# Optimization experiments

Hardware: AMD Instinct MI355X
Metric: run time of the kernel (lower is better)

## Reference

```python
import jax, jax.numpy as jnp
import numpy as np

B, T_ENC, T_DEC = 32, 600, 600
TARGET, PRE, HID, ATT, LOCF, LOCK, POSTH = 80, 256, 512, 128, 32, 31, 512


def _lstm(x, h, c, wih, whh, bih, bhh):
    g = x @ wih.T + bih + h @ whh.T + bhh
    i, f, gg, o = jnp.split(g, 4, axis=-1)
    c2 = jax.nn.sigmoid(f) * c + jax.nn.sigmoid(i) * jnp.tanh(gg)
    return jax.nn.sigmoid(o) * jnp.tanh(c2), c2


def _conv1d(x, w, pad):
    return jax.lax.conv_general_dilated(x, w, (1,), [(pad, pad)], dimension_numbers=('NCH', 'OIH', 'NCH'))


def setup_inputs():
    key = jax.random.key(0)
    ks = jax.random.split(key, 24)
    rn = lambda k, s: jax.random.normal(k, s, dtype=jnp.float32) * 0.05
    return {
        'encoder_inputs': jax.random.normal(ks[0], (B, T_ENC, HID), dtype=jnp.float32),
        'decoder_inputs': jax.random.normal(ks[1], (B, T_DEC, TARGET), dtype=jnp.float32),
        'pn_w1': rn(ks[2], (PRE, TARGET)), 'pn_b1': jnp.zeros((PRE,), jnp.float32),
        'pn_w2': rn(ks[3], (PRE, PRE)), 'pn_b2': jnp.zeros((PRE,), jnp.float32),
        'arnn_wih': rn(ks[4], (4 * HID, PRE + HID)), 'arnn_whh': rn(ks[5], (4 * HID, HID)),
        'arnn_bih': jnp.zeros((4 * HID,), jnp.float32), 'arnn_bhh': jnp.zeros((4 * HID,), jnp.float32),
        'drnn_wih': rn(ks[6], (4 * HID, 2 * HID)), 'drnn_whh': rn(ks[7], (4 * HID, HID)),
        'drnn_bih': jnp.zeros((4 * HID,), jnp.float32), 'drnn_bhh': jnp.zeros((4 * HID,), jnp.float32),
        'mem_w': rn(ks[8], (ATT, HID)), 'mem_b': jnp.zeros((ATT,), jnp.float32),
        'q_w': rn(ks[9], (ATT, HID)),
        'loc_conv_w': rn(ks[10], (LOCF, 2, LOCK)),
        'loc_fc_w': rn(ks[11], (ATT, LOCF)),
        'v_w': rn(ks[12], (1, ATT)),
        'proj_w': rn(ks[13], (TARGET, 2 * HID)),
        'post_w0': rn(ks[14], (POSTH, TARGET, 5)), 'post_b0': jnp.zeros((POSTH,), jnp.float32),
        'post_w1': rn(ks[15], (POSTH, POSTH, 5)), 'post_b1': jnp.zeros((POSTH,), jnp.float32),
        'post_w2': rn(ks[16], (POSTH, POSTH, 5)), 'post_b2': jnp.zeros((POSTH,), jnp.float32),
        'post_w3': rn(ks[17], (POSTH, POSTH, 5)), 'post_b3': jnp.zeros((POSTH,), jnp.float32),
        'post_w4': rn(ks[18], (TARGET, POSTH, 5)), 'post_b4': jnp.zeros((TARGET,), jnp.float32),
    }


def _forward(encoder_inputs, decoder_inputs, pn_w1, pn_b1, pn_w2, pn_b2,
             arnn_wih, arnn_whh, arnn_bih, arnn_bhh,
             drnn_wih, drnn_whh, drnn_bih, drnn_bhh,
             mem_w, mem_b, q_w, loc_conv_w, loc_fc_w, v_w, proj_w,
             post_w0, post_b0, post_w1, post_b1, post_w2, post_b2,
             post_w3, post_b3, post_w4, post_b4):
    Bsz, Tdec, tdim = decoder_inputs.shape
    Tenc = encoder_inputs.shape[1]
    dt = decoder_inputs.dtype
    # prenet on [go_frame; decoder_inputs]; loop consumes frames 0..Tdec-1
    go = jnp.zeros((Bsz, 1, tdim), dt)
    dec = jnp.concatenate([go, decoder_inputs], axis=1)
    pre = jax.nn.relu(jax.nn.relu(dec @ pn_w1.T + pn_b1) @ pn_w2.T + pn_b2)
    xs = jnp.transpose(pre[:, :Tdec], (1, 0, 2))  # (Tdec, B, PRE)
    proc_mem = encoder_inputs @ mem_w.T + mem_b  # (B, Tenc, ATT)
    z = jnp.zeros((Bsz, HID), dt)
    zw = jnp.zeros((Bsz, Tenc), dt)
    carry0 = (z, z, z, z, z, zw, zw)

    def step(carry, dec_in):
        ah, ac, dh, dc, ctx, w, wcum = carry
        ah, ac = _lstm(jnp.concatenate([dec_in, ctx], -1), ah, ac, arnn_wih, arnn_whh, arnn_bih, arnn_bhh)
        wcat = jnp.stack([w, wcum], axis=1)  # (B, 2, Tenc)
        loc = _conv1d(wcat, loc_conv_w, (LOCK - 1) // 2)  # (B, LOCF, Tenc)
        loc = jnp.einsum('bct,ac->bta', loc, loc_fc_w)  # (B, Tenc, ATT)
        q = ah @ q_w.T  # (B, ATT)
        e = jnp.tanh(q[:, None, :] + proc_mem + loc) @ v_w[0]  # (B, Tenc)
        w2 = jax.nn.softmax(e, axis=-1)
        ctx2 = jnp.einsum('bt,bte->be', w2, encoder_inputs)
        wcum2 = wcum + w2
        dh2, dc2 = _lstm(jnp.concatenate([ah, ctx2], -1), dh, dc, drnn_wih, drnn_whh, drnn_bih, drnn_bhh)
        mel = jnp.concatenate([dh2, ctx2], -1) @ proj_w.T  # (B, TARGET)
        return (ah, ac, dh2, dc2, ctx2, w2, wcum2), mel

    _, mels = jax.lax.scan(step, carry0, xs)
    mel_out = jnp.transpose(mels, (1, 0, 2))  # (B, Tdec, TARGET)
    # postnet: 5 conv1d layers, tanh on all but last (eval mode, no dropout)
    y = jnp.transpose(mel_out, (0, 2, 1))  # (B, TARGET, Tdec)
    y = jnp.tanh(_conv1d(y, post_w0, 2) + post_b0[None, :, None])
    y = jnp.tanh(_conv1d(y, post_w1, 2) + post_b1[None, :, None])
    y = jnp.tanh(_conv1d(y, post_w2, 2) + post_b2[None, :, None])
    y = jnp.tanh(_conv1d(y, post_w3, 2) + post_b3[None, :, None])
    y = _conv1d(y, post_w4, 2) + post_b4[None, :, None]  # (B, TARGET, Tdec)
    return mel_out + jnp.transpose(y, (0, 2, 1))


def reference(encoder_inputs, decoder_inputs, pn_w1, pn_b1, pn_w2, pn_b2,
              arnn_wih, arnn_whh, arnn_bih, arnn_bhh,
              drnn_wih, drnn_whh, drnn_bih, drnn_bhh,
              mem_w, mem_b, q_w, loc_conv_w, loc_fc_w, v_w, proj_w,
              post_w0, post_b0, post_w1, post_b1, post_w2, post_b2,
              post_w3, post_b3, post_w4, post_b4):
    return _forward(encoder_inputs, decoder_inputs, pn_w1, pn_b1, pn_w2, pn_b2,
                    arnn_wih, arnn_whh, arnn_bih, arnn_bhh,
                    drnn_wih, drnn_whh, drnn_bih, drnn_bhh,
                    mem_w, mem_b, q_w, loc_conv_w, loc_fc_w, v_w, proj_w,
                    post_w0, post_b0, post_w1, post_b1, post_w2, post_b2,
                    post_w3, post_b3, post_w4, post_b4)
```

## Files before the change

kernel.cpp:

```cpp
#include <hip/hip_runtime.h>
#include <hip/hip_bf16.h>

typedef __hip_bfloat16 bf16;

#define NB   32
#define TE   600
#define TD   600
#define TGT  80
#define PREN 256
#define HID  512
#define ATTD 128
#define LF   32
#define LK   31
#define PH   512

__device__ __forceinline__ float b2f(bf16 x){ return __bfloat162float(x); }

__device__ __forceinline__ void ld8bf(const bf16* p, float* o){
  const uint4 u = *(const uint4*)p;
  o[0]=__uint_as_float(u.x<<16); o[1]=__uint_as_float(u.x&0xFFFF0000u);
  o[2]=__uint_as_float(u.y<<16); o[3]=__uint_as_float(u.y&0xFFFF0000u);
  o[4]=__uint_as_float(u.z<<16); o[5]=__uint_as_float(u.z&0xFFFF0000u);
  o[6]=__uint_as_float(u.w<<16); o[7]=__uint_as_float(u.w&0xFFFF0000u);
}

__device__ __forceinline__ void ld8f(const float* p, float* o){
  float4 a=*(const float4*)p, b=*(const float4*)(p+4);
  o[0]=a.x;o[1]=a.y;o[2]=a.z;o[3]=a.w;
  o[4]=b.x;o[5]=b.y;o[6]=b.z;o[7]=b.w;
}

__device__ __forceinline__ float dot8(const float* w, const float* z){
  return w[0]*z[0]+w[1]*z[1]+w[2]*z[2]+w[3]*z[3]
       + w[4]*z[4]+w[5]*z[5]+w[6]*z[6]+w[7]*z[7];
}

__device__ __forceinline__ float sigm(float x){ return 1.f/(1.f+__expf(-x)); }
__device__ __forceinline__ float tanhfast(float x){
  float e = __expf(2.f*x);
  return 1.f - 2.f/(e+1.f);
}

__global__ __launch_bounds__(256) void k_prenet(const float* __restrict__ dec,
    const float* __restrict__ w1, const float* __restrict__ b1,
    const float* __restrict__ w2, const float* __restrict__ b2,
    bf16* __restrict__ XS)
{
  int t = blockIdx.x, tid = threadIdx.x;
  __shared__ __align__(16) float fr[NB*TGT];
  __shared__ __align__(16) float h1[NB*PREN];
  for (int i=tid;i<NB*TGT;i+=256){
    int b=i/TGT,c=i%TGT;
    fr[b*TGT+c] = (t==0)?0.f:dec[((size_t)b*TD+(t-1))*TGT+c];
  }
  __syncthreads();
  {
    int oc=tid; float bb=b1[oc];
    const float* wr = w1 + (size_t)oc*TGT;
    for (int b=0;b<NB;b++){
      float acc=bb;
      for (int k=0;k<TGT;k+=8){
        float wv[8]; ld8f(wr+k,wv);
        acc += dot8(wv, fr + b*TGT + k);
      }
      h1[b*PREN+oc]=fmaxf(acc,0.f);
    }
  }
  __syncthreads();
  {
    int oc=tid; float bb=b2[oc];
    const float* wr = w2 + (size_t)oc*PREN;
    for (int b=0;b<NB;b++){
      float acc=bb;
      for (int k=0;k<PREN;k+=8){
        float wv[8]; ld8f(wr+k,wv);
        acc += dot8(wv, h1 + b*PREN + k);
      }
      XS[((size_t)t*NB+b)*PREN+oc]=__float2bfloat16(fmaxf(acc,0.f));
    }
  }
}

__global__ __launch_bounds__(256) void k_procmem(const float* __restrict__ enc,
    const float* __restrict__ mw, const float* __restrict__ mb, bf16* __restrict__ PM)
{
  int t=blockIdx.x, tid=threadIdx.x;
  __shared__ __align__(16) float xe[16*HID];
  int a = tid & 127, bh = tid >> 7;
  float bb = mb[a];
  const float* wr = mw + (size_t)a*HID;
  for (int half=0; half<2; half++){
    __syncthreads();
    for (int i=tid;i<16*HID;i+=256){
      int bl=i>>9, h=i&511;
      xe[i] = enc[((size_t)(half*16+bl)*TE + t)*HID + h];
    }
    __syncthreads();
    for (int bl=bh*8; bl<bh*8+8; bl++){
      float acc=bb;
      for (int k=0;k<HID;k+=8){
        float wv[8]; ld8f(wr+k,wv);
        acc += dot8(wv, xe + bl*HID + k);
      }
      PM[((size_t)(half*16+bl)*TE + t)*ATTD + a] = __float2bfloat16(acc);
    }
  }
}

__global__ __launch_bounds__(256) void k_att1m(
    const float* __restrict__ AHn, const float* __restrict__ W,
    const float* __restrict__ WCUM, const bf16* __restrict__ PM,
    float* __restrict__ E,
    const float* __restrict__ qw, const float* __restrict__ convw,
    const float* __restrict__ fcw, const float* __restrict__ vw,
    const float* __restrict__ DHp, const float* __restrict__ CTX,
    const float* __restrict__ projw, float* __restrict__ MEL, int t)
{
  int blk = blockIdx.x, tid = threadIdx.x;
  int b = blk & 31, chunk = blk >> 5;
  __shared__ __align__(16) float wpad[632], wcpad[632], qs[128], vv[128];
  __shared__ __align__(16) float fcs[128*33];
  __shared__ __align__(16) float cw0[32*31], cw1[32*31];
  __shared__ __align__(16) float convb[4][32];
  for (int i=tid;i<630;i+=256){
    wpad[i]  = (i>=15 && i<615) ? W[(size_t)b*TE + i-15] : 0.f;
    wcpad[i] = (i>=15 && i<615) ? WCUM[(size_t)b*TE + i-15] : 0.f;
  }
  for (int i=tid;i<32*31;i+=256){
    int c=i/31, k=i-c*31;
    cw0[i] = convw[c*62 + k];
    cw1[i] = convw[c*62 + 31 + k];
  }
  for (int i=tid;i<128*33;i+=256){
    int a=i/33, c=i-a*33;
    fcs[i] = (c<32)? fcw[a*32+c] : 0.f;
  }
  if (tid < 128){
    vv[tid] = vw[tid];
    const float* qr = qw + (size_t)tid*HID;
    const float* ah = AHn + b*HID;
    float acc = 0.f;
    for (int k=0;k<HID;k+=8){
      float wv[8]; ld8f(qr+k,wv);
      acc += dot8(wv, ah+k);
    }
    qs[tid] = acc;
  }
  if (t>0 && tid<40){
    int md = blk*5 + (tid>>3);
    int jb = tid&7;
    int o = md%TGT, bb = md/TGT;
    const float* pw = projw + (size_t)o*1024;
    const float* dh = DHp + bb*HID;
    const float* c2 = CTX + bb*HID;
    float a=0.f;
    for (int i=0;i<16;i++){
      int k = jb*128 + i*8;
      const float* zp = (k<512)? dh+k : c2+(k-512);
      float z[8]; ld8f(zp,z);
      float wv[8]; ld8f(pw+k,wv);
      a += dot8(wv,z);
    }
    a += __shfl_xor(a,1); a += __shfl_xor(a,2); a += __shfl_xor(a,4);
    if (jb==0) MEL[((size_t)bb*TD + (t-1))*TGT + o] = a;
  }
  __syncthreads();
  int wid = tid>>6, lane = tid&63;
  int tbase = chunk*38;
  int tend  = min(tbase+38, TE);
  for (int it=0; it<10; it++){
    int tt = tbase + it*4 + wid;
    bool act = (tt < tend);
    if (act && lane < 32){
      int c = lane; float s = 0.f;
      for (int k=0;k<LK;k++)
        s += cw0[c*31+k]*wpad[tt+k] + cw1[c*31+k]*wcpad[tt+k];
      convb[wid][c] = s;
    }
    __syncthreads();
    if (act){
      float part = 0.f;
      #pragma unroll
      for (int half=0; half<2; half++){
        int a = lane + half*64;
        float loc = 0.f;
        #pragma unroll
        for (int c=0;c<32;c++) loc += fcs[a*33+c]*convb[wid][c];
        float x = qs[a] + b2f(PM[((size_t)b*TE + tt)*ATTD + a]) + loc;
        part += vv[a]*tanhfast(x);
      }
      for (int off=1; off<64; off<<=1) part += __shfl_xor(part, off);
      if (lane==0) E[(size_t)b*TE + tt] = part;
    }
    __syncthreads();
  }
}

__global__ __launch_bounds__(256) void k_att23(const float* __restrict__ E,
    float* __restrict__ W, float* __restrict__ WCUM,
    const float* __restrict__ enc, float* __restrict__ CTX)
{
  int blk=blockIdx.x, tid=threadIdx.x;
  int b = blk>>4, q16 = blk&15;
  __shared__ __align__(16) float wl[600];
  __shared__ float part[256];
  __shared__ float red[4];
  float e0[3]; float mx=-1e30f;
  #pragma unroll
  for (int r=0;r<3;r++){
    int i=tid+r*256;
    float v=(i<TE)? E[(size_t)b*TE+i] : -1e30f;
    e0[r]=v; mx=fmaxf(mx,v);
  }
  for (int off=1;off<64;off<<=1) mx=fmaxf(mx,__shfl_xor(mx,off));
  if ((tid&63)==0) red[tid>>6]=mx;
  __syncthreads();
  float m=fmaxf(fmaxf(red[0],red[1]),fmaxf(red[2],red[3]));
  float ex[3]; float s=0.f;
  #pragma unroll
  for (int r=0;r<3;r++){
    int i=tid+r*256;
    ex[r]=(i<TE)? __expf(e0[r]-m) : 0.f;
    s+=ex[r];
  }
  for (int off=1;off<64;off<<=1) s+=__shfl_xor(s,off);
  __syncthreads();
  if ((tid&63)==0) red[tid>>6]=s;
  __syncthreads();
  float inv=1.f/(red[0]+red[1]+red[2]+red[3]);
  #pragma unroll
  for (int r=0;r<3;r++){
    int i=tid+r*256;
    if (i<TE){
      float w2=ex[r]*inv;
      wl[i]=w2;
      if (q16==0){
        W[(size_t)b*TE+i]=w2;
        WCUM[(size_t)b*TE+i]+=w2;
      }
    }
  }
  __syncthreads();
  {
    int hl=tid&31, tj=tid>>5;
    int h=q16*32+hl;
    const float* ep = enc + ((size_t)b*TE)*HID + h;
    int tb_=tj*75;
    float a0=0.f,a1=0.f,a2=0.f;
    for (int u=0;u<25;u++){
      int tt=tb_+u*3;
      a0 += wl[tt  ]*ep[(size_t)(tt  )*HID];
      a1 += wl[tt+1]*ep[(size_t)(tt+1)*HID];
      a2 += wl[tt+2]*ep[(size_t)(tt+2)*HID];
    }
    part[tid]=a0+a1+a2;
  }
  __syncthreads();
  if (tid<32){
    float v=0.f;
    #pragma unroll
    for (int k=0;k<8;k++) v += part[tid + 32*k];
    CTX[b*HID + q16*32 + tid]=v;
  }
}

__global__ __launch_bounds__(256) void k_lstmAD(
    const bf16* __restrict__ XS, const float* __restrict__ CTX,
    float* __restrict__ AH0, float* __restrict__ AH1, float* __restrict__ AC,
    float* __restrict__ DH0, float* __restrict__ DH1, float* __restrict__ DC,
    const float* __restrict__ awih, const float* __restrict__ awhh,
    const float* __restrict__ abih, const float* __restrict__ abhh,
    const float* __restrict__ dwih, const float* __restrict__ dwhh,
    const float* __restrict__ dbih, const float* __restrict__ dbhh,
    int t)
{
  int blk=blockIdx.x, tid=threadIdx.x;
  int b=tid>>3, j=tid&7;
  if (blk<512){
    int s = t+1;
    if (s>=TD) return;
    int cell = blk;
    const bf16* xs = XS + ((size_t)s*NB+b)*PREN;
    const float* cx = CTX + b*HID;
    const float* hr = ((s&1)?AH1:AH0) + b*HID;
    float* hw = (s&1)?AH0:AH1;
    float acc[4];
    #pragma unroll
    for (int q=0;q<4;q++) acc[q]=0.f;
    for (int i=0;i<20;i++){
      int k8=i*64+j*8;
      float z[8];
      if (k8<256) ld8bf(xs+k8,z);
      else ld8f((k8<768)? cx+(k8-256) : hr+(k8-768), z);
      #pragma unroll
      for (int g=0;g<4;g++){
        int row = g*HID + cell;
        const float* wp = (k8<768) ? (awih + (size_t)row*768 + k8)
                                   : (awhh + (size_t)row*HID + (k8-768));
        float wv[8]; ld8f(wp,wv);
        acc[g] += dot8(wv,z);
      }
    }
    #pragma unroll
    for (int q=0;q<4;q++){
      acc[q] += __shfl_xor(acc[q],1);
      acc[q] += __shfl_xor(acc[q],2);
      acc[q] += __shfl_xor(acc[q],4);
    }
    if (j==0){
      float g0=acc[0]+abih[0*HID+cell]+abhh[0*HID+cell];
      float g1=acc[1]+abih[1*HID+cell]+abhh[1*HID+cell];
      float g2=acc[2]+abih[2*HID+cell]+abhh[2*HID+cell];
      float g3=acc[3]+abih[3*HID+cell]+abhh[3*HID+cell];
      float c2 = sigm(g1)*AC[b*HID+cell] + sigm(g0)*tanhfast(g2);
      AC[b*HID+cell]=c2;
      hw[b*HID+cell]=sigm(g3)*tanhfast(c2);
    }
  } else {
    if (t<0) return;
    int cell = blk-512;
    const float* ah  = ((t&1)?AH0:AH1) + b*HID;
    const float* cx  = CTX + b*HID;
    const float* dhr = ((t&1)?DH1:DH0) + b*HID;
    float* dhw = (t&1)?DH0:DH1;
    float acc[4];
    #pragma unroll
    for (int q=0;q<4;q++) acc[q]=0.f;
    for (int i=0;i<24;i++){
      int k8=i*64+j*8;
      const float* zp = (k8<512)? ah+k8 : (k8<1024)? cx+(k8-512) : dhr+(k8-1024);
      float z[8]; ld8f(zp,z);
      #pragma unroll
      for (int g=0;g<4;g++){
        int row = g*HID + cell;
        const float* wp = (k8<1024) ? (dwih + (size_t)row*1024 + k8)
                                    : (dwhh + (size_t)row*HID + (k8-1024));
        float wv[8]; ld8f(wp,wv);
        acc[g] += dot8(wv,z);
      }
    }
    #pragma unroll
    for (int q=0;q<4;q++){
      acc[q] += __shfl_xor(acc[q],1);
      acc[q] += __shfl_xor(acc[q],2);
      acc[q] += __shfl_xor(acc[q],4);
    }
    if (j==0){
      float g0=acc[0]+dbih[0*HID+cell]+dbhh[0*HID+cell];
      float g1=acc[1]+dbih[1*HID+cell]+dbhh[1*HID+cell];
      float g2=acc[2]+dbih[2*HID+cell]+dbhh[2*HID+cell];
      float g3=acc[3]+dbih[3*HID+cell]+dbhh[3*HID+cell];
      float c2 = sigm(g1)*DC[b*HID+cell] + sigm(g0)*tanhfast(g2);
      DC[b*HID+cell]=c2;
      dhw[b*HID+cell]=sigm(g3)*tanhfast(c2);
    }
  }
}

__global__ __launch_bounds__(256) void k_melfinal(const float* __restrict__ DH,
    const float* __restrict__ CTX, const float* __restrict__ projw, float* __restrict__ MEL)
{
  int gid=blockIdx.x*256+threadIdx.x;
  if (gid>=NB*TGT) return;
  int o=gid%TGT, b=gid/TGT;
  const float* pw=projw+(size_t)o*1024;
  float a=0.f;
  for (int k=0;k<HID;k+=8){
    float wv[8]; ld8f(pw+k,wv);
    a += dot8(wv, DH + b*HID + k);
  }
  for (int k=0;k<HID;k+=8){
    float wv[8]; ld8f(pw+512+k,wv);
    a += dot8(wv, CTX + b*HID + k);
  }
  MEL[((size_t)b*TD+599)*TGT+o]=a;
}

__global__ __launch_bounds__(256) void k_conv(
    const void* __restrict__ inv_, bf16* __restrict__ out,
    const float* __restrict__ w, const float* __restrict__ bias,
    int IC, int OC, int mel_in, int do_tanh, int b0)
{
  __shared__ __align__(16) float xs[256*36];
  int bl=blockIdx.x, bg=b0+bl, oct=blockIdx.y, t0=blockIdx.z*32, tid=threadIdx.x;
  int oc = oct*256 + tid;
  float acc[32];
  #pragma unroll
  for (int q=0;q<32;q++) acc[q]=0.f;
  int nch=(IC+255)/256;
  const float* inf_ = (const float*)inv_;
  const bf16*  inb_ = (const bf16*)inv_;
  for (int ch=0;ch<nch;ch++){
    int icb=ch*256, icn=min(256,IC-icb);
    __syncthreads();
    for (int i=tid;i<icn*36;i+=256){
      int icl=i/36, tt=i-icl*36;
      int tg=t0+tt-2;
      float v=0.f;
      if (tg>=0 && tg<TD){
        int ic=icb+icl;
        v = mel_in ? inf_[((size_t)bg*TD+tg)*TGT+ic]
                   : b2f(inb_[((size_t)bl*IC+ic)*TD+tg]);
      }
      xs[i]=v;
    }
    __syncthreads();
    if (oc<OC){
      const float* wp = w + ((size_t)oc*IC+icb)*5;
      for (int ic=0;ic<icn;ic++){
        float xw[36];
        #pragma unroll
        for (int q=0;q<9;q++) ((float4*)xw)[q]=((const float4*)(xs+ic*36))[q];
        float wk0=wp[ic*5  ],wk1=wp[ic*5+1],wk2=wp[ic*5+2],
              wk3=wp[ic*5+3],wk4=wp[ic*5+4];
        #pragma unroll
        for (int tt=0;tt<32;tt++)
          acc[tt] += wk0*xw[tt]+wk1*xw[tt+1]+wk2*xw[tt+2]+wk3*xw[tt+3]+wk4*xw[tt+4];
      }
    }
  }
  if (oc<OC){
    float bv=bias[oc];
    for (int tt=0;tt<32;tt++){
      int tg=t0+tt;
      if (tg<TD){
        float v=acc[tt]+bv;
        if (do_tanh) v=tanhfast(v);
        out[((size_t)bl*OC+oc)*TD+tg]=__float2bfloat16(v);
      }
    }
  }
}

__global__ __launch_bounds__(256) void k_conv_last(
    const bf16* __restrict__ in, const float* __restrict__ w,
    const float* __restrict__ bias, float* __restrict__ outp, int b0)
{
  __shared__ __align__(16) float xs[256*36];
  int bl=blockIdx.x, bg=b0+bl, t0=blockIdx.z*32, tid=threadIdx.x;
  int oc = tid;
  float acc[32];
  #pragma unroll
  for (int q=0;q<32;q++) acc[q]=0.f;
  for (int ch=0;ch<2;ch++){
    int icb=ch*256;
    __syncthreads();
    for (int i=tid;i<256*36;i+=256){
      int icl=i/36, tt=i-icl*36;
      int tg=t0+tt-2;
      float v=0.f;
      if (tg>=0 && tg<TD){
        int ic=icb+icl;
        v = b2f(in[((size_t)bl*PH+ic)*TD+tg]);
      }
      xs[i]=v;
    }
    __syncthreads();
    if (oc<TGT){
      const float* wp = w + ((size_t)oc*PH+icb)*5;
      for (int ic=0;ic<256;ic++){
        float xw[36];
        #pragma unroll
        for (int q=0;q<9;q++) ((float4*)xw)[q]=((const float4*)(xs+ic*36))[q];
        float wk0=wp[ic*5  ],wk1=wp[ic*5+1],wk2=wp[ic*5+2],
              wk3=wp[ic*5+3],wk4=wp[ic*5+4];
        #pragma unroll
        for (int tt=0;tt<32;tt++)
          acc[tt] += wk0*xw[tt]+wk1*xw[tt+1]+wk2*xw[tt+2]+wk3*xw[tt+3]+wk4*xw[tt+4];
      }
    }
  }
  if (oc<TGT){
    float bv=bias[oc];
    for (int tt=0;tt<32;tt++){
      int tg=t0+tt;
      if (tg<TD){
        size_t idx=((size_t)bg*TD+tg)*TGT+oc;
        outp[idx]=acc[tt]+bv+outp[idx];
      }
    }
  }
}

extern "C" void kernel_launch(void* const* d_in, const int* in_sizes, int n_in,
                              void* d_out, int out_size, void* d_ws, size_t ws_size,
                              hipStream_t stream)
{
  const float* enc =(const float*)d_in[0];
  const float* dec =(const float*)d_in[1];
  const float* pw1 =(const float*)d_in[2];  const float* pb1=(const float*)d_in[3];
  const float* pw2 =(const float*)d_in[4];  const float* pb2=(const float*)d_in[5];
  const float* awih=(const float*)d_in[6];  const float* awhh=(const float*)d_in[7];
  const float* abih=(const float*)d_in[8];  const float* abhh=(const float*)d_in[9];
  const float* dwih=(const float*)d_in[10]; const float* dwhh=(const float*)d_in[11];
  const float* dbih=(const float*)d_in[12]; const float* dbhh=(const float*)d_in[13];
  const float* memw=(const float*)d_in[14]; const float* memb=(const float*)d_in[15];
  const float* qw  =(const float*)d_in[16];
  const float* lcw =(const float*)d_in[17];
  const float* lfw =(const float*)d_in[18];
  const float* vw  =(const float*)d_in[19];
  const float* pjw =(const float*)d_in[20];
  const float* cwt0=(const float*)d_in[21]; const float* cbt0=(const float*)d_in[22];
  const float* cwt1=(const float*)d_in[23]; const float* cbt1=(const float*)d_in[24];
  const float* cwt2=(const float*)d_in[25]; const float* cbt2=(const float*)d_in[26];
  const float* cwt3=(const float*)d_in[27]; const float* cbt3=(const float*)d_in[28];
  const float* cwt4=(const float*)d_in[29]; const float* cbt4=(const float*)d_in[30];
  float* MEL = (float*)d_out;
  (void)in_sizes; (void)n_in; (void)out_size; (void)ws_size;

  char* base=(char*)d_ws;
  const size_t XS_B = (size_t)TD*NB*PREN*2;
  const size_t PM_B = (size_t)NB*TE*ATTD*2;
  const size_t HB   = (size_t)NB*HID*4;
  const size_t WB   = (size_t)NB*TE*4;
  bf16* XSb = (bf16*)base;
  bf16* PMb = (bf16*)(base + XS_B);
  char* sbase = base + XS_B + PM_B;
  float* AH0b=(float*)(sbase+0*HB);
  float* AH1b=(float*)(sbase+1*HB);
  float* ACb =(float*)(sbase+2*HB);
  float* DH0b=(float*)(sbase+3*HB);
  float* DH1b=(float*)(sbase+4*HB);
  float* DCb =(float*)(sbase+5*HB);
  float* CTX =(float*)(sbase+6*HB);
  float* Wb  =(float*)(sbase+7*HB);
  float* WC  =(float*)(sbase+7*HB+WB);
  float* Eb  =(float*)(sbase+7*HB+2*WB);
  const int G = 8;
  const size_t PBc_B = (size_t)G*PH*TD*2;
  bf16* PB0 = (bf16*)base;
  bf16* PB1 = (bf16*)(base + PBc_B);

  hipMemsetAsync(sbase, 0, 7*HB+3*WB, stream);

  k_prenet<<<TD,256,0,stream>>>(dec,pw1,pb1,pw2,pb2,XSb);
  k_procmem<<<TE,256,0,stream>>>(enc,memw,memb,PMb);

  k_lstmAD<<<1024,256,0,stream>>>(XSb,CTX,AH0b,AH1b,ACb,DH0b,DH1b,DCb,
                                  awih,awhh,abih,abhh,dwih,dwhh,dbih,dbhh,-1);
  for (int t=0;t<TD;t++){
    const float* AHn = (t&1)? AH0b : AH1b;
    const float* DHp = (t&1)? DH1b : DH0b;
    k_att1m<<<512,256,0,stream>>>(AHn,Wb,WC,PMb,Eb,qw,lcw,lfw,vw,DHp,CTX,pjw,MEL,t);
    k_att23<<<512,256,0,stream>>>(Eb,Wb,WC,enc,CTX);
    k_lstmAD<<<1024,256,0,stream>>>(XSb,CTX,AH0b,AH1b,ACb,DH0b,DH1b,DCb,
                                    awih,awhh,abih,abhh,dwih,dwhh,dbih,dbhh,t);
  }
  k_melfinal<<<10,256,0,stream>>>(DH0b,CTX,pjw,MEL);

  for (int c=0;c<NB/G;c++){
    int b0=c*G;
    k_conv<<<dim3(G,2,19),256,0,stream>>>(MEL,PB0,cwt0,cbt0,TGT,PH,1,1,b0);
    k_conv<<<dim3(G,2,19),256,0,stream>>>(PB0,PB1,cwt1,cbt1,PH,PH,0,1,b0);
    k_conv<<<dim3(G,2,19),256,0,stream>>>(PB1,PB0,cwt2,cbt2,PH,PH,0,1,b0);
    k_conv<<<dim3(G,2,19),256,0,stream>>>(PB0,PB1,cwt3,cbt3,PH,PH,0,1,b0);
    k_conv_last<<<dim3(G,1,19),256,0,stream>>>(PB1,cwt4,cbt4,MEL,b0);
  }
}
```

Measured before the change: 63.23 ms.

## Restructure decoder step into two kernels, precomputing location features alongside LSTMs

The per-step attention is reorganized from three launches to two. The location conv and FC for the next step are computed into a bf16 LOC buffer by extra blocks in the LSTM kernel, which depend only on the already-updated attention weights. Energy, softmax and context are fused into one kernel per (batch, quarter-of-hidden) block, and the mel projection runs in separate blocks of that kernel. CTX is double-buffered so the new context and the previous one can coexist. This removes one launch per step and takes the location computation off the critical path, at the cost of redundant energy/softmax computation across the four blocks of each batch row, bf16 rounding of the location term, and fewer blocks in the attention kernel.

Measured after the change: 99.67 ms. 57.6% more time.

```diff
diff --git a/kernel.cpp b/kernel.cpp
--- a/kernel.cpp
+++ b/kernel.cpp
@@ -107,109 +107,80 @@
   }
 }
 
-__global__ __launch_bounds__(256) void k_att1m(
-    const float* __restrict__ AHn, const float* __restrict__ W,
-    const float* __restrict__ WCUM, const bf16* __restrict__ PM,
-    float* __restrict__ E,
-    const float* __restrict__ qw, const float* __restrict__ convw,
-    const float* __restrict__ fcw, const float* __restrict__ vw,
-    const float* __restrict__ DHp, const float* __restrict__ CTX,
+__global__ __launch_bounds__(256) void k_bc(
+    const float* __restrict__ AH, const bf16* __restrict__ PM,
+    const bf16* __restrict__ LOC, const float* __restrict__ enc,
+    const float* __restrict__ qw, const float* __restrict__ vw,
+    float* __restrict__ W, float* __restrict__ WCUM, float* __restrict__ CTXw,
+    const float* __restrict__ DHp, const float* __restrict__ CTXp,
     const float* __restrict__ projw, float* __restrict__ MEL, int t)
 {
-  int blk = blockIdx.x, tid = threadIdx.x;
-  int b = blk & 31, chunk = blk >> 5;
-  __shared__ __align__(16) float wpad[632], wcpad[632], qs[128], vv[128];
-  __shared__ __align__(16) float fcs[128*33];
-  __shared__ __align__(16) float cw0[32*31], cw1[32*31];
-  __shared__ __align__(16) float convb[4][32];
-  for (int i=tid;i<630;i+=256){
-    wpad[i]  = (i>=15 && i<615) ? W[(size_t)b*TE + i-15] : 0.f;
-    wcpad[i] = (i>=15 && i<615) ? WCUM[(size_t)b*TE + i-15] : 0.f;
-  }
-  for (int i=tid;i<32*31;i+=256){
-    int c=i/31, k=i-c*31;
-    cw0[i] = convw[c*62 + k];
-    cw1[i] = convw[c*62 + 31 + k];
-  }
-  for (int i=tid;i<128*33;i+=256){
-    int a=i/33, c=i-a*33;
-    fcs[i] = (c<32)? fcw[a*32+c] : 0.f;
-  }
+  int blk=blockIdx.x, tid=threadIdx.x;
+  if (blk>=128){
+    if (t==0) return;
+    int b = blk-128;
+    const float* dh = DHp + b*HID;
+    const float* c2 = CTXp + b*HID;
+    #pragma unroll
+    for (int pass=0; pass<3; ++pass){
+      int o = pass*32 + (tid>>3);
+      if (o<TGT){
+        int j = tid&7;
+        const float* pw = projw + (size_t)o*1024;
+        float a=0.f;
+        for (int i=0;i<16;i++){
+          int k = j*128 + i*8;
+          const float* zp = (k<512)? dh+k : c2+(k-512);
+          float z[8]; ld8f(zp,z);
+          float wv[8]; ld8f(pw+k,wv);
+          a += dot8(wv,z);
+        }
+        a += __shfl_xor(a,1); a += __shfl_xor(a,2); a += __shfl_xor(a,4);
+        if (j==0) MEL[((size_t)b*TD + (t-1))*TGT + o] = a;
+      }
+    }
+    return;
+  }
+  int b = blk>>2, k4 = blk&3;
+  __shared__ float qs[128], vv[128];
+  __shared__ __align__(16) float el[608], wl[608];
+  __shared__ float part[256];
+  __shared__ float red[4];
   if (tid < 128){
     vv[tid] = vw[tid];
     const float* qr = qw + (size_t)tid*HID;
-    const float* ah = AHn + b*HID;
+    const float* ah = AH + b*HID;
     float acc = 0.f;
-    for (int k=0;k<HID;k+=8){
-      float wv[8]; ld8f(qr+k,wv);
-      acc += dot8(wv, ah+k);
+    for (int kk=0;kk<HID;kk+=8){
+      float wv2[8]; ld8f(qr+kk,wv2);
+      acc += dot8(wv2, ah+kk);
     }
     qs[tid] = acc;
   }
-  if (t>0 && tid<40){
-    int md = blk*5 + (tid>>3);
-    int jb = tid&7;
-    int o = md%TGT, bb = md/TGT;
-    const float* pw = projw + (size_t)o*1024;
-    const float* dh = DHp + bb*HID;
-    const float* c2 = CTX + bb*HID;
-    float a=0.f;
-    for (int i=0;i<16;i++){
-      int k = jb*128 + i*8;
-      const float* zp = (k<512)? dh+k : c2+(k-512);
-      float z[8]; ld8f(zp,z);
-      float wv[8]; ld8f(pw+k,wv);
-      a += dot8(wv,z);
-    }
-    a += __shfl_xor(a,1); a += __shfl_xor(a,2); a += __shfl_xor(a,4);
-    if (jb==0) MEL[((size_t)bb*TD + (t-1))*TGT + o] = a;
-  }
-  __syncthreads();
-  int wid = tid>>6, lane = tid&63;
-  int tbase = chunk*38;
-  int tend  = min(tbase+38, TE);
-  for (int it=0; it<10; it++){
-    int tt = tbase + it*4 + wid;
-    bool act = (tt < tend);
-    if (act && lane < 32){
-      int c = lane; float s = 0.f;
-      for (int k=0;k<LK;k++)
-        s += cw0[c*31+k]*wpad[tt+k] + cw1[c*31+k]*wcpad[tt+k];
-      convb[wid][c] = s;
-    }
-    __syncthreads();
-    if (act){
-      float part = 0.f;
+  __syncthreads();
+  {
+    int wv_=tid>>6, lane=tid&63;
+    float q0 = qs[2*lane], q1 = qs[2*lane+1];
+    float v0 = vv[2*lane], v1 = vv[2*lane+1];
+    const unsigned* pmp = (const unsigned*)(PM + (size_t)b*TE*ATTD) + lane;
+    const unsigned* lcp = (const unsigned*)(LOC + (size_t)b*TE*ATTD) + lane;
+    for (int tt=wv_; tt<TE; tt+=4){
+      unsigned pm2 = pmp[(size_t)tt*64];
+      unsigned lc2 = lcp[(size_t)tt*64];
+      float x0 = q0 + __uint_as_float(pm2<<16) + __uint_as_float(lc2<<16);
+      float x1 = q1 + __uint_as_float(pm2&0xFFFF0000u) + __uint_as_float(lc2&0xFFFF0000u);
+      float p = v0*tanhfast(x0) + v1*tanhfast(x1);
       #pragma unroll
-      for (int half=0; half<2; half++){
-        int a = lane + half*64;
-        float loc = 0.f;
-        #pragma unroll
-        for (int c=0;c<32;c++) loc += fcs[a*33+c]*convb[wid][c];
-        float x = qs[a] + b2f(PM[((size_t)b*TE + tt)*ATTD + a]) + loc;
-        part += vv[a]*tanhfast(x);
-      }
-      for (int off=1; off<64; off<<=1) part += __shfl_xor(part, off);
-      if (lane==0) E[(size_t)b*TE + tt] = part;
-    }
-    __syncthreads();
-  }
-}
-
-__global__ __launch_bounds__(256) void k_att23(const float* __restrict__ E,
-    float* __restrict__ W, float* __restrict__ WCUM,
-    const float* __restrict__ enc, float* __restrict__ CTX)
-{
-  int blk=blockIdx.x, tid=threadIdx.x;
-  int b = blk>>4, q16 = blk&15;
-  __shared__ __align__(16) float wl[600];
-  __shared__ float part[256];
-  __shared__ float red[4];
+      for (int off=1; off<64; off<<=1) p += __shfl_xor(p, off);
+      if (lane==0) el[tt] = p;
+    }
+  }
+  __syncthreads();
   float e0[3]; float mx=-1e30f;
   #pragma unroll
   for (int r=0;r<3;r++){
     int i=tid+r*256;
-    float v=(i<TE)? E[(size_t)b*TE+i] : -1e30f;
+    float v=(i<TE)? el[i] : -1e30f;
     e0[r]=v; mx=fmaxf(mx,v);
   }
   for (int off=1;off<64;off<<=1) mx=fmaxf(mx,__shfl_xor(mx,off));
@@ -234,7 +205,7 @@
     if (i<TE){
       float w2=ex[r]*inv;
       wl[i]=w2;
-      if (q16==0){
+      if (k4==0){
         W[(size_t)b*TE+i]=w2;
         WCUM[(size_t)b*TE+i]+=w2;
       }
@@ -242,32 +213,31 @@
   }
   __syncthreads();
   {
-    int hl=tid&31, tj=tid>>5;
-    int h=q16*32+hl;
+    int hl = tid&127, tl = tid>>7;
+    int h = k4*128 + hl;
     const float* ep = enc + ((size_t)b*TE)*HID + h;
-    int tb_=tj*75;
     float a0=0.f,a1=0.f,a2=0.f;
-    for (int u=0;u<25;u++){
-      int tt=tb_+u*3;
+    for (int u=0; u<100; ++u){
+      int tt = tl + u*6;
       a0 += wl[tt  ]*ep[(size_t)(tt  )*HID];
-      a1 += wl[tt+1]*ep[(size_t)(tt+1)*HID];
-      a2 += wl[tt+2]*ep[(size_t)(tt+2)*HID];
+      a1 += wl[tt+2]*ep[(size_t)(tt+2)*HID];
+      a2 += wl[tt+4]*ep[(size_t)(tt+4)*HID];
     }
     part[tid]=a0+a1+a2;
   }
   __syncthreads();
-  if (tid<32){
-    float v=0.f;
-    #pragma unroll
-    for (int k=0;k<8;k++) v += part[tid + 32*k];
-    CTX[b*HID + q16*32 + tid]=v;
-  }
-}
-
-__global__ __launch_bounds__(256) void k_lstmAD(
-    const bf16* __restrict__ XS, const float* __restrict__ CTX,
-    float* __restrict__ AH0, float* __restrict__ AH1, float* __restrict__ AC,
-    float* __restrict__ DH0, float* __restrict__ DH1, float* __restrict__ DC,
+  if (tid<128)
+    CTXw[b*HID + k4*128 + tid] = part[tid] + part[128+tid];
+}
+
+__global__ __launch_bounds__(256) void k_ea(
+    const bf16* __restrict__ XS,
+    const float* __restrict__ CTXt, const float* __restrict__ AHt,
+    float* __restrict__ AHw, float* __restrict__ AC,
+    const float* __restrict__ DHp, float* __restrict__ DHw, float* __restrict__ DC,
+    const float* __restrict__ W, const float* __restrict__ WCUM,
+    const float* __restrict__ convw, const float* __restrict__ fcw,
+    bf16* __restrict__ LOC,
     const float* __restrict__ awih, const float* __restrict__ awhh,
     const float* __restrict__ abih, const float* __restrict__ abhh,
     const float* __restrict__ dwih, const float* __restrict__ dwhh,
@@ -275,15 +245,14 @@
     int t)
 {
   int blk=blockIdx.x, tid=threadIdx.x;
-  int b=tid>>3, j=tid&7;
   if (blk<512){
     int s = t+1;
     if (s>=TD) return;
+    int b=tid>>3, j=tid&7;
     int cell = blk;
     const bf16* xs = XS + ((size_t)s*NB+b)*PREN;
-    const float* cx = CTX + b*HID;
-    const float* hr = ((s&1)?AH1:AH0) + b*HID;
-    float* hw = (s&1)?AH0:AH1;
+    const float* cx = CTXt + b*HID;
+    const float* hr = AHt + b*HID;
     float acc[4];
     #pragma unroll
     for (int q=0;q<4;q++) acc[q]=0.f;
@@ -314,15 +283,15 @@
       float g3=acc[3]+abih[3*HID+cell]+abhh[3*HID+cell];
       float c2 = sigm(g1)*AC[b*HID+cell] + sigm(g0)*tanhfast(g2);
       AC[b*HID+cell]=c2;
-      hw[b*HID+cell]=sigm(g3)*tanhfast(c2);
-    }
-  } else {
+      AHw[b*HID+cell]=sigm(g3)*tanhfast(c2);
+    }
+  } else if (blk<1024){
     if (t<0) return;
+    int b=tid>>3, j=tid&7;
     int cell = blk-512;
-    const float* ah  = ((t&1)?AH0:AH1) + b*HID;
-    const float* cx  = CTX + b*HID;
-    const float* dhr = ((t&1)?DH1:DH0) + b*HID;
-    float* dhw = (t&1)?DH0:DH1;
+    const float* ah  = AHt + b*HID;
+    const float* cx  = CTXt + b*HID;
+    const float* dhr = DHp + b*HID;
     float acc[4];
     #pragma unroll
     for (int q=0;q<4;q++) acc[q]=0.f;
@@ -352,7 +321,57 @@
       float g3=acc[3]+dbih[3*HID+cell]+dbhh[3*HID+cell];
       float c2 = sigm(g1)*DC[b*HID+cell] + sigm(g0)*tanhfast(g2);
       DC[b*HID+cell]=c2;
-      dhw[b*HID+cell]=sigm(g3)*tanhfast(c2);
+      DHw[b*HID+cell]=sigm(g3)*tanhfast(c2);
+    }
+  } else {
+    if (t+1>=TD) return;
+    int idx = blk-1024;
+    int b = idx>>3, s8 = idx&7;
+    int tb = s8*75;
+    __shared__ __align__(16) float wp_[112], wc_[112];
+    __shared__ __align__(16) float cw0[32*31], cw1[32*31];
+    __shared__ __align__(16) float cb[75*32];
+    __shared__ __align__(16) float fcs[128*33];
+    if (tid<105){
+      int g = tb-15+tid;
+      bool ok = (g>=0 && g<TE);
+      wp_[tid] = ok ? W[(size_t)b*TE+g] : 0.f;
+      wc_[tid] = ok ? WCUM[(size_t)b*TE+g] : 0.f;
+    }
+    for (int i=tid;i<32*31;i+=256){
+      int c=i/31, k=i-c*31;
+      cw0[i] = convw[c*62 + k];
+      cw1[i] = convw[c*62 + 31 + k];
+    }
+    for (int i=tid;i<128*33;i+=256){
+      int a=i/33, c=i-a*33;
+      fcs[i] = (c<32)? fcw[a*32+c] : 0.f;
+    }
+    __syncthreads();
+    for (int i=tid;i<75*32;i+=256){
+      int tt=i>>5, c=i&31;
+      float s=0.f;
+      for (int k=0;k<LK;k++)
+        s += cw0[c*31+k]*wp_[tt+k] + cw1[c*31+k]*wc_[tt+k];
+      cb[tt*32+c]=s;
+    }
+    __syncthreads();
+    {
+      int lane = tid&63, tl = tid>>6;
+      int a0 = 2*lane;
+      for (int tt=tl; tt<75; tt+=4){
+        float l0=0.f, l1=0.f;
+        const float* cbr = cb + tt*32;
+        #pragma unroll
+        for (int c=0;c<32;c++){
+          float cv = cbr[c];
+          l0 += fcs[a0*33+c]*cv;
+          l1 += fcs[(a0+1)*33+c]*cv;
+        }
+        size_t off = ((size_t)b*TE + tb + tt)*ATTD + a0;
+        LOC[off]   = __float2bfloat16(l0);
+        LOC[off+1] = __float2bfloat16(l1);
+      }
     }
   }
 }
@@ -513,40 +532,49 @@
   const size_t PM_B = (size_t)NB*TE*ATTD*2;
   const size_t HB   = (size_t)NB*HID*4;
   const size_t WB   = (size_t)NB*TE*4;
+  const size_t LOC_B= (size_t)NB*TE*ATTD*2;
   bf16* XSb = (bf16*)base;
   bf16* PMb = (bf16*)(base + XS_B);
   char* sbase = base + XS_B + PM_B;
-  float* AH0b=(float*)(sbase+0*HB);
-  float* AH1b=(float*)(sbase+1*HB);
+  float* AHb[2], *DHb[2], *CTXb[2];
+  AHb[0] =(float*)(sbase+0*HB);
+  AHb[1] =(float*)(sbase+1*HB);
   float* ACb =(float*)(sbase+2*HB);
-  float* DH0b=(float*)(sbase+3*HB);
-  float* DH1b=(float*)(sbase+4*HB);
+  DHb[0] =(float*)(sbase+3*HB);
+  DHb[1] =(float*)(sbase+4*HB);
   float* DCb =(float*)(sbase+5*HB);
-  float* CTX =(float*)(sbase+6*HB);
-  float* Wb  =(float*)(sbase+7*HB);
-  float* WC  =(float*)(sbase+7*HB+WB);
-  float* Eb  =(float*)(sbase+7*HB+2*WB);
+  CTXb[0]=(float*)(sbase+6*HB);
+  CTXb[1]=(float*)(sbase+7*HB);
+  float* Wb  =(float*)(sbase+8*HB);
+  float* WC  =(float*)(sbase+8*HB+WB);
+  bf16*  LOCb=(bf16*)(sbase+8*HB+2*WB);
   const int G = 8;
   const size_t PBc_B = (size_t)G*PH*TD*2;
   bf16* PB0 = (bf16*)base;
   bf16* PB1 = (bf16*)(base + PBc_B);
 
-  hipMemsetAsync(sbase, 0, 7*HB+3*WB, stream);
+  hipMemsetAsync(sbase, 0, 8*HB+2*WB, stream);
 
   k_prenet<<<TD,256,0,stream>>>(dec,pw1,pb1,pw2,pb2,XSb);
   k_procmem<<<TE,256,0,stream>>>(enc,memw,memb,PMb);
 
-  k_lstmAD<<<1024,256,0,stream>>>(XSb,CTX,AH0b,AH1b,ACb,DH0b,DH1b,DCb,
-                                  awih,awhh,abih,abhh,dwih,dwhh,dbih,dbhh,-1);
+  k_ea<<<1280,256,0,stream>>>(XSb, CTXb[1], AHb[1], AHb[0], ACb,
+                              DHb[0], DHb[1], DCb, Wb, WC, lcw, lfw, LOCb,
+                              awih,awhh,abih,abhh,dwih,dwhh,dbih,dbhh, -1);
   for (int t=0;t<TD;t++){
-    const float* AHn = (t&1)? AH0b : AH1b;
-    const float* DHp = (t&1)? DH1b : DH0b;
-    k_att1m<<<512,256,0,stream>>>(AHn,Wb,WC,PMb,Eb,qw,lcw,lfw,vw,DHp,CTX,pjw,MEL,t);
-    k_att23<<<512,256,0,stream>>>(Eb,Wb,WC,enc,CTX);
-    k_lstmAD<<<1024,256,0,stream>>>(XSb,CTX,AH0b,AH1b,ACb,DH0b,DH1b,DCb,
-                                    awih,awhh,abih,abhh,dwih,dwhh,dbih,dbhh,t);
-  }
-  k_melfinal<<<10,256,0,stream>>>(DH0b,CTX,pjw,MEL);
+    float* AHt  = AHb[t&1];
+    float* AHw  = AHb[(t+1)&1];
+    float* DHp  = DHb[(t+1)&1];
+    float* DHw  = DHb[t&1];
+    float* CTXt = CTXb[t&1];
+    float* CTXp = CTXb[(t+1)&1];
+    k_bc<<<160,256,0,stream>>>(AHt, PMb, LOCb, enc, qw, vw,
+                               Wb, WC, CTXt, DHp, CTXp, pjw, MEL, t);
+    k_ea<<<1280,256,0,stream>>>(XSb, CTXt, AHt, AHw, ACb,
+                                DHp, DHw, DCb, Wb, WC, lcw, lfw, LOCb,
+                                awih,awhh,abih,abhh,dwih,dwhh,dbih,dbhh, t);
+  }
+  k_melfinal<<<10,256,0,stream>>>(DHb[1],CTXb[1],pjw,MEL);
 
   for (int c=0;c<NB/G;c++){
     int b0=c*G;
```
